# Optimization experiments

Measured on AMD Instinct MI355X. Metric: run time of the kernel, lower is better.

The kernel has to match this reference:

```python
import jax, jax.numpy as jnp
import numpy as np

N = 50000   # nodes of the target node type
E = 800000  # edges per incoming edge type (avg degree 16)
D = 128     # in == hidden == out channels (required by the module's pooling layer)


def sage_mean(x, edge_index, Wl, bl, Wr):
    """PyG SAGEConv with mean aggregation: lin_l(mean_j x_j) + lin_r(x_i).
    Note: per the original code, sources are gathered from the TARGET node
    feature table (x_input = x_dict[tgt_node_type])."""
    src, tgt = edge_index[0], edge_index[1]
    msg = x[src]                                                   # [E, D] gather
    agg = jax.ops.segment_sum(msg, tgt, num_segments=x.shape[0])   # [N, D] scatter-add
    cnt = jax.ops.segment_sum(jnp.ones((edge_index.shape[1],), x.dtype), tgt,
                              num_segments=x.shape[0])             # [N] degree
    agg = agg / jnp.maximum(cnt, 1.0)[:, None]                     # mean; 0 for isolated nodes
    return agg @ Wl + bl + x @ Wr                                  # [N, D]


def setup_inputs() -> dict:
    key = jax.random.key(0)
    ks = jax.random.split(key, 6)
    s = 1.0 / np.sqrt(D)
    x = jax.random.normal(ks[0], (N, D), jnp.float32)
    edge_index_a = jax.random.randint(ks[1], (2, E), 0, N)
    edge_index_b = jax.random.randint(ks[2], (2, E), 0, N)
    Wl = jax.random.normal(ks[3], (D, D), jnp.float32) * s
    Wr = jax.random.normal(ks[4], (D, D), jnp.float32) * s
    bl = jnp.zeros((D,), jnp.float32)
    Wp = jax.random.normal(ks[5], (D, D), jnp.float32) * s
    bp = jnp.zeros((D,), jnp.float32)
    return {"x": x, "Wl": Wl, "bl": bl, "Wr": Wr, "Wp": Wp, "bp": bp,
            "edge_index_a": edge_index_a, "edge_index_b": edge_index_b}


def reference(x, Wl, bl, Wr, Wp, bp, edge_index_a, edge_index_b):
    # One SAGEConv encoder + pooling Linear shared across incoming edge types,
    # softmax per edge type, then mean over edge types (torch.stack(...).mean(0)).
    outs = []
    for ei in (edge_index_a, edge_index_b):
        h = sage_mean(x, ei, Wl, bl, Wr)            # [N, D]
        outs.append(jax.nn.softmax(h @ Wp + bp, axis=-1))
    return (outs[0] + outs[1]) * 0.5                # [N, D]
```

## Files before the change

### kernel.cpp

```cpp
#include <hip/hip_runtime.h>
#include <math.h>

constexpr int D    = 128;
constexpr int BT   = 128;
constexpr int TILE = 4096;
constexpr int CE   = 256;

using bf16x8 = __attribute__((ext_vector_type(8))) short;
using f32x4  = __attribute__((ext_vector_type(4))) float;
using f32x2  = __attribute__((ext_vector_type(2))) float;
#define MFMA16 __builtin_amdgcn_mfma_f32_16x16x32_bf16

__device__ __forceinline__ unsigned short f2bf(float f) {
    unsigned u = __builtin_bit_cast(unsigned, f);
    u = (u + 0x7FFF + ((u >> 16) & 1)) >> 16;
    return (unsigned short)u;
}

__global__ __launch_bounds__(256)
void wprod_kernel(const float* __restrict__ Wl, const float* __restrict__ Wr,
                  const float* __restrict__ Wp,
                  const float* __restrict__ bl, const float* __restrict__ bp,
                  unsigned short* __restrict__ WlpB, unsigned short* __restrict__ WrpB,
                  float* __restrict__ cvec)
{
    __shared__ float wm[128 * 129];
    __shared__ float wpc[128 * 16];

    const int bid = blockIdx.x;
    const int m   = bid >> 3;
    const int cg  = bid & 7;
    const int c0  = cg * 16;
    const float* Wm = m ? Wr : Wl;
    unsigned short* OB = m ? WrpB : WlpB;
    const int t = threadIdx.x;

    for (int i = t; i < 128 * 128; i += 256) {
        int r = i >> 7, k = i & 127;
        wm[r * 129 + k] = Wm[i];
    }
    for (int i = t; i < 2048; i += 256) {
        int k = i >> 4, col = i & 15;
        wpc[i] = Wp[k * 128 + c0 + col];
    }
    __syncthreads();

    const int r = t >> 1;
    const int h = (t & 1) * 8;
    float acc[8];
    #pragma unroll
    for (int j = 0; j < 8; ++j) acc[j] = 0.f;

    for (int k = 0; k < 128; ++k) {
        float wv = wm[r * 129 + k];
        #pragma unroll
        for (int j = 0; j < 8; ++j) acc[j] += wv * wpc[k * 16 + h + j];
    }

    const int kt = r >> 5, lhi = (r >> 3) & 3, jj = r & 7;
    #pragma unroll
    for (int j = 0; j < 8; ++j) {
        int l = lhi * 16 + h + j;
        OB[((size_t)(kt * 8 + cg) * 64 + l) * 8 + jj] = f2bf(acc[j]);
    }

    if (m == 0 && t < 16) {
        int c = c0 + t;
        float s = bp[c];
        for (int k = 0; k < 128; ++k) s += bl[k] * wpc[k * 16 + t];
        cvec[c] = s;
    }
}

__global__ __launch_bounds__(256)
void prep_kernel(const int* __restrict__ ea, int Ea,
                 const int* __restrict__ eb, int Eb,
                 unsigned int* __restrict__ ent_a, int* __restrict__ cnt_a,
                 unsigned int* __restrict__ ent_b, int* __restrict__ cnt_b,
                 int NBKT, int CAP, int GA)
{
    __shared__ int hist[512];
    __shared__ int base[512];

    const int bid = blockIdx.x;
    const int t   = threadIdx.x;

    const int type = (bid >= GA);
    const int* e   = type ? eb : ea;
    const int  E   = type ? Eb : Ea;
    unsigned int* ent = type ? ent_b : ent_a;
    int* cnt          = type ? cnt_b : cnt_a;
    const int i0 = (bid - type * GA) * TILE;

    for (int h = t; h < NBKT; h += 256) hist[h] = 0;
    __syncthreads();

    int tgts[16];
    #pragma unroll
    for (int j = 0; j < 16; ++j) {
        int i = i0 + j * 256 + t;
        tgts[j] = (i < E) ? e[(size_t)E + i] : -1;
        if (tgts[j] >= 0) atomicAdd(&hist[tgts[j] >> 7], 1);
    }
    __syncthreads();

    for (int h = t; h < NBKT; h += 256) {
        base[h] = (hist[h] > 0) ? atomicAdd(&cnt[h], hist[h]) : 0;
        hist[h] = 0;
    }
    __syncthreads();

    #pragma unroll
    for (int j = 0; j < 16; ++j) {
        int i = i0 + j * 256 + t;
        if (tgts[j] >= 0) {
            int b   = tgts[j] >> 7;
            int pos = base[b] + atomicAdd(&hist[b], 1);
            if (pos < CAP)
                ent[(size_t)b * CAP + pos] = ((unsigned)e[i] << 7) | (tgts[j] & 127);
        }
    }
}

__global__ __launch_bounds__(512)
void sort_kernel(const unsigned int* __restrict__ ent_a, const int* __restrict__ cnt_a,
                 const unsigned int* __restrict__ ent_b, const int* __restrict__ cnt_b,
                 unsigned short* __restrict__ srcl_g, int* __restrict__ off_g,
                 int NBKT, int CAP)
{
    extern __shared__ __align__(16) char smem_raw[];
    int* tmp  = (int*)smem_raw;
    int* off  = tmp + CAP;
    int* cur  = off + BT + 1;
    int* wtot = cur + BT;
    unsigned short* srcl = (unsigned short*)(wtot + 2);

    const int bid  = blockIdx.x;
    const int type = (bid >= NBKT);
    const int k    = bid - type * NBKT;
    const unsigned int* ent = type ? ent_b : ent_a;
    const int cnt = min((type ? cnt_b : cnt_a)[k], CAP);

    const int t = threadIdx.x, l = t & 63, w = t >> 6;

    if (t < BT) off[t] = 0;
    __syncthreads();

    for (int i = t; i < cnt; i += 512) {
        unsigned e = ent[(size_t)k * CAP + i];
        tmp[i] = (int)e;
        atomicAdd(&off[e & (BT - 1)], 1);
    }
    __syncthreads();

    int v = 0, s = 0;
    if (t < BT) {
        v = off[t]; s = v;
        #pragma unroll
        for (int o = 1; o < 64; o <<= 1) {
            int u = __shfl_up(s, o, 64);
            if (l >= o) s += u;
        }
        if (l == 63) wtot[w] = s;
    }
    __syncthreads();
    if (t < BT) {
        int ex = ((w == 1) ? wtot[0] : 0) + s - v;
        off[t] = ex; cur[t] = ex;
    }
    if (t == 0) off[BT] = wtot[0] + wtot[1];
    __syncthreads();

    for (int i = t; i < cnt; i += 512) {
        unsigned e = (unsigned)tmp[i];
        int pos = atomicAdd(&cur[e & (BT - 1)], 1);
        srcl[pos] = (unsigned short)(e >> 7);
    }
    __syncthreads();

    for (int i = t; i < cnt; i += 512)
        srcl_g[(size_t)bid * CAP + i] = srcl[i];
    if (t <= BT)
        off_g[(size_t)bid * (BT + 1) + t] = off[t];
}

__global__ __launch_bounds__(256)
void gemmz_kernel(const float* __restrict__ x,
                  const unsigned short* __restrict__ WlpB,
                  const unsigned short* __restrict__ WrpB,
                  const float* __restrict__ cvec,
                  unsigned short* __restrict__ zl, unsigned short* __restrict__ zr,
                  int N)
{
    const int t = threadIdx.x, w = t >> 6, l = t & 63;
    const int q = l & 15, kg = l >> 4;
    const int node0 = blockIdx.x * 64 + w * 16;
    const int arow = min(node0 + q, N - 1);

    const float4* xp = reinterpret_cast<const float4*>(x + (size_t)arow * D);
    bf16x8 fx[4];
    #pragma unroll
    for (int kt = 0; kt < 4; ++kt) {
        float4 a = xp[kt * 8 + kg * 2];
        float4 b = xp[kt * 8 + kg * 2 + 1];
        bf16x8 f;
        f[0] = (short)f2bf(a.x); f[1] = (short)f2bf(a.y);
        f[2] = (short)f2bf(a.z); f[3] = (short)f2bf(a.w);
        f[4] = (short)f2bf(b.x); f[5] = (short)f2bf(b.y);
        f[6] = (short)f2bf(b.z); f[7] = (short)f2bf(b.w);
        fx[kt] = f;
    }

    #pragma unroll
    for (int nt = 0; nt < 8; ++nt) {
        f32x4 cl = {0.f, 0.f, 0.f, 0.f};
        f32x4 cr = {0.f, 0.f, 0.f, 0.f};
        #pragma unroll
        for (int kt = 0; kt < 4; ++kt) {
            const size_t fo = ((size_t)(kt * 8 + nt) * 64 + l) * 8;
            bf16x8 wl = *reinterpret_cast<const bf16x8*>(WlpB + fo);
            bf16x8 wr = *reinterpret_cast<const bf16x8*>(WrpB + fo);
            cl = MFMA16(fx[kt], wl, cl, 0, 0, 0);
            cr = MFMA16(fx[kt], wr, cr, 0, 0, 0);
        }
        float cv = cvec[nt * 16 + q];
        const int sidx = nt >> 1;
        const int cin  = (nt & 1) * 16 + q;
        #pragma unroll
        for (int r = 0; r < 4; ++r) {
            int grow = node0 + kg * 4 + r;
            if (grow < N) {
                zl[((size_t)sidx * (N + 1) + grow) * 32 + cin] = f2bf(cl[r]);
                zr[(size_t)grow * D + nt * 16 + q]             = f2bf(cr[r] + cv);
            }
        }
    }
}

__global__ __launch_bounds__(256)
void gather_kernel(const unsigned short* __restrict__ zl,
                   const unsigned short* __restrict__ srcl_g,
                   const int* __restrict__ off_g,
                   unsigned short* __restrict__ agg_a,
                   unsigned short* __restrict__ agg_b,
                   int N, int NBKT, int CAP)
{
    __shared__ int off[BT + 1];
    __shared__ unsigned short stage[2][CE * 32];

    const int bid   = blockIdx.x;
    const int slice = bid & 3;
    const int tb    = bid >> 2;
    const int type  = (tb >= NBKT);
    const int k     = tb - type * NBKT;

    const int t = threadIdx.x, l = t & 63, w = t >> 6;
    const int tg = l >> 3;
    const int c8 = l & 7;

    for (int i = t; i <= BT; i += 256)
        off[i] = off_g[(size_t)tb * (BT + 1) + i];
    __syncthreads();

    const int cnt = off[BT];
    const unsigned short* zs = zl + (size_t)slice * (N + 1) * 32;
    const unsigned short* sl = srcl_g + (size_t)tb * CAP;

    int myt[4], mo0[4], mo1[4];
    f32x2 accP[4], accQ[4];
    #pragma unroll
    for (int p = 0; p < 4; ++p) {
        myt[p] = p * 32 + w * 8 + tg;
        mo0[p] = off[myt[p]];
        mo1[p] = off[myt[p] + 1];
        accP[p] = f32x2{0.f, 0.f};
        accQ[p] = f32x2{0.f, 0.f};
    }

    const int nc = (cnt + CE - 1) / CE;

#define STAGE(cc, bb)                                                         \
    {                                                                         \
        const int _c0 = (cc) * CE;                                            \
        _Pragma("unroll")                                                     \
        for (int i = 0; i < 4; ++i) {                                         \
            const int el = w * 64 + i * 16 + (l >> 2);                        \
            const unsigned sid = sl[_c0 + el];                                \
            const char* g = (const char*)zs + (size_t)sid * 64 + (l & 3) * 16;\
            char* ldsb = (char*)stage[bb] + (size_t)(w * 64 + i * 16) * 64;   \
            __builtin_amdgcn_global_load_lds(                                 \
                (const __attribute__((address_space(1))) unsigned*)g,         \
                (__attribute__((address_space(3))) unsigned*)ldsb, 16, 0, 0); \
        }                                                                     \
    }

    if (nc > 0) STAGE(0, 0);

    for (int c = 0; c < nc; ++c) {
        if (c + 1 < nc) {
            STAGE(c + 1, (c + 1) & 1);
            asm volatile("s_waitcnt vmcnt(4)" ::: "memory");
        } else {
            asm volatile("s_waitcnt vmcnt(0)" ::: "memory");
        }
        __builtin_amdgcn_s_barrier();
        asm volatile("" ::: "memory");

        const int c0 = c * CE, c1 = c0 + CE;
        const unsigned short* sg = stage[c & 1];
        #pragma unroll
        for (int p = 0; p < 4; ++p) {
            const int lo = max(mo0[p], c0);
            const int hi = min(mo1[p], c1);
            int j = lo;
            for (; j + 1 < hi; j += 2) {
                uint2 v0 = *reinterpret_cast<const uint2*>(sg + (j - c0) * 32 + c8 * 4);
                uint2 v1 = *reinterpret_cast<const uint2*>(sg + (j + 1 - c0) * 32 + c8 * 4);
                f32x2 p0, q0, p1, q1;
                p0[0] = __builtin_bit_cast(float, v0.x << 16);
                p0[1] = __builtin_bit_cast(float, v0.y << 16);
                q0[0] = __builtin_bit_cast(float, v0.x & 0xffff0000u);
                q0[1] = __builtin_bit_cast(float, v0.y & 0xffff0000u);
                p1[0] = __builtin_bit_cast(float, v1.x << 16);
                p1[1] = __builtin_bit_cast(float, v1.y << 16);
                q1[0] = __builtin_bit_cast(float, v1.x & 0xffff0000u);
                q1[1] = __builtin_bit_cast(float, v1.y & 0xffff0000u);
                accP[p] += p0 + p1;
                accQ[p] += q0 + q1;
            }
            if (j < hi) {
                uint2 v0 = *reinterpret_cast<const uint2*>(sg + (j - c0) * 32 + c8 * 4);
                f32x2 p0, q0;
                p0[0] = __builtin_bit_cast(float, v0.x << 16);
                p0[1] = __builtin_bit_cast(float, v0.y << 16);
                q0[0] = __builtin_bit_cast(float, v0.x & 0xffff0000u);
                q0[1] = __builtin_bit_cast(float, v0.y & 0xffff0000u);
                accP[p] += p0;
                accQ[p] += q0;
            }
        }
        asm volatile("" ::: "memory");
        __builtin_amdgcn_s_barrier();
    }
#undef STAGE

    unsigned short* agg = (type ? agg_b : agg_a) + (size_t)slice * N * 32;
    #pragma unroll
    for (int p = 0; p < 4; ++p) {
        const int n = k * BT + myt[p];
        const int deg = mo1[p] - mo0[p];
        if (n < N) {
            const float r = 1.0f / fmaxf((float)deg, 1.0f);
            uint2 o;
            o.x = ((unsigned)f2bf(accQ[p][0] * r) << 16) | f2bf(accP[p][0] * r);
            o.y = ((unsigned)f2bf(accQ[p][1] * r) << 16) | f2bf(accP[p][1] * r);
            *reinterpret_cast<uint2*>(agg + (size_t)n * 32 + c8 * 4) = o;
        }
    }
}

__global__ __launch_bounds__(256)
void epi_kernel(const unsigned short* __restrict__ agg_a,
                const unsigned short* __restrict__ agg_b,
                const unsigned short* __restrict__ zr,
                float* __restrict__ out, int N)
{
    const int t = threadIdx.x;
    const int n = blockIdx.x * 16 + (t >> 4);
    const int c = t & 15;
    if (n >= N) return;

    const int s = c >> 2;
    const size_t aoff = ((size_t)s * N + n) * 32 + (c & 3) * 8;
    uint4 va = *reinterpret_cast<const uint4*>(agg_a + aoff);
    uint4 vb = *reinterpret_cast<const uint4*>(agg_b + aoff);
    uint4 vz = *reinterpret_cast<const uint4*>(zr + (size_t)n * D + c * 8);

    unsigned ua[4] = {va.x, va.y, va.z, va.w};
    unsigned ub[4] = {vb.x, vb.y, vb.z, vb.w};
    unsigned uz[4] = {vz.x, vz.y, vz.z, vz.w};

    float la[8], lb[8];
    #pragma unroll
    for (int d = 0; d < 4; ++d) {
        float z0 = __builtin_bit_cast(float, uz[d] << 16);
        float z1 = __builtin_bit_cast(float, uz[d] & 0xffff0000u);
        la[2*d]   = __builtin_bit_cast(float, ua[d] << 16) + z0;
        la[2*d+1] = __builtin_bit_cast(float, ua[d] & 0xffff0000u) + z1;
        lb[2*d]   = __builtin_bit_cast(float, ub[d] << 16) + z0;
        lb[2*d+1] = __builtin_bit_cast(float, ub[d] & 0xffff0000u) + z1;
    }

    float ma = -INFINITY, mb = -INFINITY;
    #pragma unroll
    for (int j = 0; j < 8; ++j) { ma = fmaxf(ma, la[j]); mb = fmaxf(mb, lb[j]); }
    #pragma unroll
    for (int o = 1; o < 16; o <<= 1) {
        ma = fmaxf(ma, __shfl_xor(ma, o, 64));
        mb = fmaxf(mb, __shfl_xor(mb, o, 64));
    }
    float sa = 0.f, sb = 0.f;
    #pragma unroll
    for (int j = 0; j < 8; ++j) {
        la[j] = __expf(la[j] - ma); sa += la[j];
        lb[j] = __expf(lb[j] - mb); sb += lb[j];
    }
    #pragma unroll
    for (int o = 1; o < 16; o <<= 1) {
        sa += __shfl_xor(sa, o, 64);
        sb += __shfl_xor(sb, o, 64);
    }
    const float ra = 0.5f / sa, rb = 0.5f / sb;

    float4 o0, o1;
    o0.x = la[0]*ra + lb[0]*rb; o0.y = la[1]*ra + lb[1]*rb;
    o0.z = la[2]*ra + lb[2]*rb; o0.w = la[3]*ra + lb[3]*rb;
    o1.x = la[4]*ra + lb[4]*rb; o1.y = la[5]*ra + lb[5]*rb;
    o1.z = la[6]*ra + lb[6]*rb; o1.w = la[7]*ra + lb[7]*rb;
    float* op = out + (size_t)n * D + c * 8;
    *reinterpret_cast<float4*>(op)     = o0;
    *reinterpret_cast<float4*>(op + 4) = o1;
}

extern "C" void kernel_launch(void* const* d_in, const int* in_sizes, int n_in,
                              void* d_out, int out_size, void* d_ws, size_t ws_size,
                              hipStream_t stream)
{
    const float* x  = (const float*)d_in[0];
    const float* Wl = (const float*)d_in[1];
    const float* bl = (const float*)d_in[2];
    const float* Wr = (const float*)d_in[3];
    const float* Wp = (const float*)d_in[4];
    const float* bp = (const float*)d_in[5];
    const int*   ea = (const int*)d_in[6];
    const int*   eb = (const int*)d_in[7];

    const int N  = in_sizes[0] / D;
    const int Ea = in_sizes[6] / 2;
    const int Eb = in_sizes[7] / 2;

    const int NBKT = (N + BT - 1) / BT;
    const int Emax = Ea > Eb ? Ea : Eb;
    int CAP = (int)(((long long)Emax * BT / N) * 5 / 4 + 128);
    CAP = (CAP + 7) & ~7;

    unsigned int* ent_a = (unsigned int*)d_ws;
    unsigned int* ent_b = ent_a + (size_t)NBKT * CAP;
    int* cnt_a = (int*)(ent_b + (size_t)NBKT * CAP);
    int* cnt_b = cnt_a + NBKT;
    int* off_g = cnt_b + NBKT;
    float* cvec = (float*)(off_g + (size_t)2 * NBKT * (BT + 1));
    uintptr_t p = (uintptr_t)(cvec + 128);
    p = (p + 15) & ~(uintptr_t)15;
    unsigned short* srcl_g = (unsigned short*)p;
    unsigned short* zl     = srcl_g + (size_t)2 * NBKT * CAP + 512;
    unsigned short* zr     = zl + (size_t)4 * (N + 1) * 32;
    unsigned short* agg_a  = zr + (size_t)N * D;
    unsigned short* agg_b  = agg_a + (size_t)N * D;
    unsigned short* WlpB   = agg_b + (size_t)N * D;
    unsigned short* WrpB   = WlpB + D * D;

    hipMemsetAsync(cnt_a, 0, sizeof(int) * 2 * (size_t)NBKT, stream);

    wprod_kernel<<<16, 256, 0, stream>>>(Wl, Wr, Wp, bl, bp, WlpB, WrpB, cvec);

    const int GA = (Ea + TILE - 1) / TILE;
    const int GB = (Eb + TILE - 1) / TILE;
    prep_kernel<<<GA + GB, 256, 0, stream>>>(ea, Ea, eb, Eb,
                                             ent_a, cnt_a, ent_b, cnt_b,
                                             NBKT, CAP, GA);

    const int smem_sort = CAP * 6 + (BT + 1 + BT + 2) * 4 + 16;
    sort_kernel<<<2 * NBKT, 512, smem_sort, stream>>>(
        ent_a, cnt_a, ent_b, cnt_b, srcl_g, off_g, NBKT, CAP);

    gemmz_kernel<<<(N + 63) / 64, 256, 0, stream>>>(
        x, WlpB, WrpB, cvec, zl, zr, N);

    gather_kernel<<<8 * NBKT, 256, 0, stream>>>(
        zl, srcl_g, off_g, agg_a, agg_b, N, NBKT, CAP);

    epi_kernel<<<(N + 15) / 16, 256, 0, stream>>>(agg_a, agg_b, zr,
                                                  (float*)d_out, N);
}
```

Before: 150.1 us.

## Shrink target buckets to 32 nodes and simplify gather to one target per thread-group

```diff
diff --git a/kernel.cpp b/kernel.cpp
--- a/kernel.cpp
+++ b/kernel.cpp
@@ -2,9 +2,9 @@
 #include <math.h>
 
 constexpr int D    = 128;
-constexpr int BT   = 128;
-constexpr int TILE = 4096;
-constexpr int CE   = 256;
+constexpr int BT   = 32;
+constexpr int TILE = 16384;
+constexpr int CE   = 128;
 
 using bf16x8 = __attribute__((ext_vector_type(8))) short;
 using f32x4  = __attribute__((ext_vector_type(4))) float;
@@ -79,8 +79,8 @@
                  unsigned int* __restrict__ ent_b, int* __restrict__ cnt_b,
                  int NBKT, int CAP, int GA)
 {
-    __shared__ int hist[512];
-    __shared__ int base[512];
+    __shared__ int hist[1600];
+    __shared__ int base[1600];
 
     const int bid = blockIdx.x;
     const int t   = threadIdx.x;
@@ -90,18 +90,14 @@
     const int  E   = type ? Eb : Ea;
     unsigned int* ent = type ? ent_b : ent_a;
     int* cnt          = type ? cnt_b : cnt_a;
-    const int i0 = (bid - type * GA) * TILE;
+    const int i0   = (bid - type * GA) * TILE;
+    const int iend = min(i0 + TILE, E);
 
     for (int h = t; h < NBKT; h += 256) hist[h] = 0;
     __syncthreads();
 
-    int tgts[16];
-    #pragma unroll
-    for (int j = 0; j < 16; ++j) {
-        int i = i0 + j * 256 + t;
-        tgts[j] = (i < E) ? e[(size_t)E + i] : -1;
-        if (tgts[j] >= 0) atomicAdd(&hist[tgts[j] >> 7], 1);
-    }
+    for (int i = i0 + t; i < iend; i += 256)
+        atomicAdd(&hist[e[(size_t)E + i] >> 5], 1);
     __syncthreads();
 
     for (int h = t; h < NBKT; h += 256) {
@@ -110,15 +106,12 @@
     }
     __syncthreads();
 
-    #pragma unroll
-    for (int j = 0; j < 16; ++j) {
-        int i = i0 + j * 256 + t;
-        if (tgts[j] >= 0) {
-            int b   = tgts[j] >> 7;
-            int pos = base[b] + atomicAdd(&hist[b], 1);
-            if (pos < CAP)
-                ent[(size_t)b * CAP + pos] = ((unsigned)e[i] << 7) | (tgts[j] & 127);
-        }
+    for (int i = i0 + t; i < iend; i += 256) {
+        int tgt = e[(size_t)E + i];
+        int b   = tgt >> 5;
+        int pos = base[b] + atomicAdd(&hist[b], 1);
+        if (pos < CAP)
+            ent[(size_t)b * CAP + pos] = ((unsigned)e[i] << 5) | (tgt & 31);
     }
 }
 
@@ -132,8 +125,7 @@
     int* tmp  = (int*)smem_raw;
     int* off  = tmp + CAP;
     int* cur  = off + BT + 1;
-    int* wtot = cur + BT;
-    unsigned short* srcl = (unsigned short*)(wtot + 2);
+    unsigned short* srcl = (unsigned short*)(cur + BT);
 
     const int bid  = blockIdx.x;
     const int type = (bid >= NBKT);
@@ -141,7 +133,7 @@
     const unsigned int* ent = type ? ent_b : ent_a;
     const int cnt = min((type ? cnt_b : cnt_a)[k], CAP);
 
-    const int t = threadIdx.x, l = t & 63, w = t >> 6;
+    const int t = threadIdx.x;
 
     if (t < BT) off[t] = 0;
     __syncthreads();
@@ -153,28 +145,23 @@
     }
     __syncthreads();
 
-    int v = 0, s = 0;
     if (t < BT) {
-        v = off[t]; s = v;
+        int v = off[t], s = v;
         #pragma unroll
-        for (int o = 1; o < 64; o <<= 1) {
+        for (int o = 1; o < 32; o <<= 1) {
             int u = __shfl_up(s, o, 64);
-            if (l >= o) s += u;
-        }
-        if (l == 63) wtot[w] = s;
-    }
-    __syncthreads();
-    if (t < BT) {
-        int ex = ((w == 1) ? wtot[0] : 0) + s - v;
+            if (t >= o) s += u;
+        }
+        int ex = s - v;
         off[t] = ex; cur[t] = ex;
-    }
-    if (t == 0) off[BT] = wtot[0] + wtot[1];
+        if (t == BT - 1) off[BT] = s;
+    }
     __syncthreads();
 
     for (int i = t; i < cnt; i += 512) {
         unsigned e = (unsigned)tmp[i];
         int pos = atomicAdd(&cur[e & (BT - 1)], 1);
-        srcl[pos] = (unsigned short)(e >> 7);
+        srcl[pos] = (unsigned short)(e >> 5);
     }
     __syncthreads();
 
@@ -266,16 +253,9 @@
     const unsigned short* zs = zl + (size_t)slice * (N + 1) * 32;
     const unsigned short* sl = srcl_g + (size_t)tb * CAP;
 
-    int myt[4], mo0[4], mo1[4];
-    f32x2 accP[4], accQ[4];
-    #pragma unroll
-    for (int p = 0; p < 4; ++p) {
-        myt[p] = p * 32 + w * 8 + tg;
-        mo0[p] = off[myt[p]];
-        mo1[p] = off[myt[p] + 1];
-        accP[p] = f32x2{0.f, 0.f};
-        accQ[p] = f32x2{0.f, 0.f};
-    }
+    const int tt = w * 8 + tg;
+    const int o0 = off[tt], o1 = off[tt + 1];
+    f32x2 aP = {0.f, 0.f}, aQ = {0.f, 0.f};
 
     const int nc = (cnt + CE - 1) / CE;
 
@@ -283,11 +263,11 @@
     {                                                                         \
         const int _c0 = (cc) * CE;                                            \
         _Pragma("unroll")                                                     \
-        for (int i = 0; i < 4; ++i) {                                         \
-            const int el = w * 64 + i * 16 + (l >> 2);                        \
+        for (int i = 0; i < 2; ++i) {                                         \
+            const int el = w * 32 + i * 16 + (l >> 2);                        \
             const unsigned sid = sl[_c0 + el];                                \
             const char* g = (const char*)zs + (size_t)sid * 64 + (l & 3) * 16;\
-            char* ldsb = (char*)stage[bb] + (size_t)(w * 64 + i * 16) * 64;   \
+            char* ldsb = (char*)stage[bb] + (size_t)(w * 32 + i * 16) * 64;   \
             __builtin_amdgcn_global_load_lds(                                 \
                 (const __attribute__((address_space(1))) unsigned*)g,         \
                 (__attribute__((address_space(3))) unsigned*)ldsb, 16, 0, 0); \
@@ -299,45 +279,42 @@
     for (int c = 0; c < nc; ++c) {
         if (c + 1 < nc) {
             STAGE(c + 1, (c + 1) & 1);
-            asm volatile("s_waitcnt vmcnt(4)" ::: "memory");
+            asm volatile("s_waitcnt vmcnt(2)" ::: "memory");
         } else {
             asm volatile("s_waitcnt vmcnt(0)" ::: "memory");
         }
         __builtin_amdgcn_s_barrier();
         asm volatile("" ::: "memory");
 
-        const int c0 = c * CE, c1 = c0 + CE;
+        const int c0 = c * CE;
         const unsigned short* sg = stage[c & 1];
-        #pragma unroll
-        for (int p = 0; p < 4; ++p) {
-            const int lo = max(mo0[p], c0);
-            const int hi = min(mo1[p], c1);
-            int j = lo;
-            for (; j + 1 < hi; j += 2) {
-                uint2 v0 = *reinterpret_cast<const uint2*>(sg + (j - c0) * 32 + c8 * 4);
-                uint2 v1 = *reinterpret_cast<const uint2*>(sg + (j + 1 - c0) * 32 + c8 * 4);
-                f32x2 p0, q0, p1, q1;
-                p0[0] = __builtin_bit_cast(float, v0.x << 16);
-                p0[1] = __builtin_bit_cast(float, v0.y << 16);
-                q0[0] = __builtin_bit_cast(float, v0.x & 0xffff0000u);
-                q0[1] = __builtin_bit_cast(float, v0.y & 0xffff0000u);
-                p1[0] = __builtin_bit_cast(float, v1.x << 16);
-                p1[1] = __builtin_bit_cast(float, v1.y << 16);
-                q1[0] = __builtin_bit_cast(float, v1.x & 0xffff0000u);
-                q1[1] = __builtin_bit_cast(float, v1.y & 0xffff0000u);
-                accP[p] += p0 + p1;
-                accQ[p] += q0 + q1;
-            }
-            if (j < hi) {
-                uint2 v0 = *reinterpret_cast<const uint2*>(sg + (j - c0) * 32 + c8 * 4);
-                f32x2 p0, q0;
-                p0[0] = __builtin_bit_cast(float, v0.x << 16);
-                p0[1] = __builtin_bit_cast(float, v0.y << 16);
-                q0[0] = __builtin_bit_cast(float, v0.x & 0xffff0000u);
-                q0[1] = __builtin_bit_cast(float, v0.y & 0xffff0000u);
-                accP[p] += p0;
-                accQ[p] += q0;
-            }
+        const int lo = max(o0, c0);
+        const int hi = min(o1, c0 + CE);
+        int j = lo;
+        for (; j + 1 < hi; j += 2) {
+            uint2 v0 = *reinterpret_cast<const uint2*>(sg + (j - c0) * 32 + c8 * 4);
+            uint2 v1 = *reinterpret_cast<const uint2*>(sg + (j + 1 - c0) * 32 + c8 * 4);
+            f32x2 p0, q0, p1, q1;
+            p0[0] = __builtin_bit_cast(float, v0.x << 16);
+            p0[1] = __builtin_bit_cast(float, v0.y << 16);
+            q0[0] = __builtin_bit_cast(float, v0.x & 0xffff0000u);
+            q0[1] = __builtin_bit_cast(float, v0.y & 0xffff0000u);
+            p1[0] = __builtin_bit_cast(float, v1.x << 16);
+            p1[1] = __builtin_bit_cast(float, v1.y << 16);
+            q1[0] = __builtin_bit_cast(float, v1.x & 0xffff0000u);
+            q1[1] = __builtin_bit_cast(float, v1.y & 0xffff0000u);
+            aP += p0 + p1;
+            aQ += q0 + q1;
+        }
+        if (j < hi) {
+            uint2 v0 = *reinterpret_cast<const uint2*>(sg + (j - c0) * 32 + c8 * 4);
+            f32x2 p0, q0;
+            p0[0] = __builtin_bit_cast(float, v0.x << 16);
+            p0[1] = __builtin_bit_cast(float, v0.y << 16);
+            q0[0] = __builtin_bit_cast(float, v0.x & 0xffff0000u);
+            q0[1] = __builtin_bit_cast(float, v0.y & 0xffff0000u);
+            aP += p0;
+            aQ += q0;
         }
         asm volatile("" ::: "memory");
         __builtin_amdgcn_s_barrier();
@@ -345,17 +322,14 @@
 #undef STAGE
 
     unsigned short* agg = (type ? agg_b : agg_a) + (size_t)slice * N * 32;
-    #pragma unroll
-    for (int p = 0; p < 4; ++p) {
-        const int n = k * BT + myt[p];
-        const int deg = mo1[p] - mo0[p];
-        if (n < N) {
-            const float r = 1.0f / fmaxf((float)deg, 1.0f);
-            uint2 o;
-            o.x = ((unsigned)f2bf(accQ[p][0] * r) << 16) | f2bf(accP[p][0] * r);
-            o.y = ((unsigned)f2bf(accQ[p][1] * r) << 16) | f2bf(accP[p][1] * r);
-            *reinterpret_cast<uint2*>(agg + (size_t)n * 32 + c8 * 4) = o;
-        }
+    const int n = k * BT + tt;
+    const int deg = o1 - o0;
+    if (n < N) {
+        const float r = 1.0f / fmaxf((float)deg, 1.0f);
+        uint2 o;
+        o.x = ((unsigned)f2bf(aQ[0] * r) << 16) | f2bf(aP[0] * r);
+        o.y = ((unsigned)f2bf(aQ[1] * r) << 16) | f2bf(aP[1] * r);
+        *reinterpret_cast<uint2*>(agg + (size_t)n * 32 + c8 * 4) = o;
     }
 }
 
@@ -470,7 +444,7 @@
                                              ent_a, cnt_a, ent_b, cnt_b,
                                              NBKT, CAP, GA);
 
-    const int smem_sort = CAP * 6 + (BT + 1 + BT + 2) * 4 + 16;
+    const int smem_sort = CAP * 6 + (BT + 1 + BT) * 4 + 16;
     sort_kernel<<<2 * NBKT, 512, smem_sort, stream>>>(
         ent_a, cnt_a, ent_b, cnt_b, srcl_g, off_g, NBKT, CAP);
 
```

After: 177.8 us. 1.18x slower.
